# Optimization experiments

Hardware: AMD Instinct MI355X
Metric: run time of the kernel (lower is better)

The kernel has to match this reference:

```python
import jax, jax.numpy as jnp
import numpy as np

B, T, E, H = 2, 2048, 1024, 16
D = E // H          # head_size = 64
DF = 4 * E          # FFN inner dim


def setup_inputs() -> dict:
    key = jax.random.key(0)
    ks = jax.random.split(key, 10)
    s = E ** -0.5
    return {
        "x":  jax.random.normal(ks[0], (B, T, E), jnp.float32),
        "Wq": jax.random.normal(ks[1], (H, E, D), jnp.float32) * s,
        "Wk": jax.random.normal(ks[2], (H, E, D), jnp.float32) * s,
        "Wv": jax.random.normal(ks[3], (H, E, D), jnp.float32) * s,
        "Wo": jax.random.normal(ks[4], (E, E), jnp.float32) * s,
        "bo": jnp.zeros((E,), jnp.float32),
        "W1": jax.random.normal(ks[5], (E, DF), jnp.float32) * s,
        "b1": jnp.zeros((DF,), jnp.float32),
        "W2": jax.random.normal(ks[6], (DF, E), jnp.float32) * (DF ** -0.5),
        "b2": jnp.zeros((E,), jnp.float32),
    }


def reference(x, Wq, Wk, Wv, Wo, bo, W1, b1, W2, b2):
    Bx, Tx, C = x.shape
    # NOTE: source scales by C**-0.5 where C = n_embed (not head_size) -- faithful.
    scale = C ** -0.5
    q = jnp.einsum('btc,hcd->bhtd', x, Wq)
    k = jnp.einsum('btc,hcd->bhtd', x, Wk)
    v = jnp.einsum('btc,hcd->bhtd', x, Wv)
    scores = jnp.einsum('bhtd,bhsd->bhts', q, k) * scale   # [B,H,T,T]
    causal = jnp.tril(jnp.ones((Tx, Tx), bool))
    scores = jnp.where(causal, scores, -jnp.inf)
    attn = jax.nn.softmax(scores, axis=-1)
    out = jnp.einsum('bhts,bhsd->bhtd', attn, v)
    out = out.transpose(0, 2, 1, 3).reshape(Bx, Tx, C)     # concat heads
    x = x + (out @ Wo + bo)                                # residual + projection
    h = jax.nn.relu(x @ W1 + b1)
    x = x + (h @ W2 + b2)                                  # residual + FFN
    return x
```

## Files before the change

### kernel.cpp

```cpp
#include <hip/hip_runtime.h>

#define B_ 2
#define T_ 2048
#define E_ 1024
#define H_ 16
#define D_ 64
#define DF_ 4096
#define M_ (B_*T_)
#define NQKV_ 3072

typedef unsigned short u16;
typedef __attribute__((ext_vector_type(8))) short short8;
typedef __attribute__((ext_vector_type(4))) float f32x4;
typedef __attribute__((ext_vector_type(16))) float f32x16;

__device__ __forceinline__ u16 f2bf(float f) {
  unsigned u = __builtin_bit_cast(unsigned, f);
  u += 0x7FFFu + ((u >> 16) & 1u);
  return (u16)(u >> 16);
}
__device__ __forceinline__ unsigned cvtpk(float a, float b) {
  unsigned r;
  asm("v_cvt_pk_bf16_f32 %0, %1, %2" : "=v"(r) : "v"(a), "v"(b));
  return r;
}
__device__ __forceinline__ float exp2a(float x) {
  float r;
  asm("v_exp_f32 %0, %1" : "=v"(r) : "v"(x));
  return r;
}
__device__ __forceinline__ float bf2f(u16 u) {
  return __builtin_bit_cast(float, (unsigned)u << 16);
}
__device__ __forceinline__ float vmax16(const f32x16& v) {
  float a0 = fmaxf(v[0], v[1]),   a1 = fmaxf(v[2], v[3]);
  float a2 = fmaxf(v[4], v[5]),   a3 = fmaxf(v[6], v[7]);
  float a4 = fmaxf(v[8], v[9]),   a5 = fmaxf(v[10], v[11]);
  float a6 = fmaxf(v[12], v[13]), a7 = fmaxf(v[14], v[15]);
  float b0 = fmaxf(a0, a1), b1 = fmaxf(a2, a3), b2 = fmaxf(a4, a5), b3 = fmaxf(a6, a7);
  return fmaxf(fmaxf(b0, b1), fmaxf(b2, b3));
}
__device__ __forceinline__ float vsum16(const f32x16& v) {
  float a0 = v[0] + v[1],   a1 = v[2] + v[3];
  float a2 = v[4] + v[5],   a3 = v[6] + v[7];
  float a4 = v[8] + v[9],   a5 = v[10] + v[11];
  float a6 = v[12] + v[13], a7 = v[14] + v[15];
  float b0 = a0 + a1, b1 = a2 + a3, b2 = a4 + a5, b3 = a6 + a7;
  return (b0 + b1) + (b2 + b3);
}

__device__ __forceinline__ void gload_lds16(const u16* g, u16* l) {
  __builtin_amdgcn_global_load_lds((const __attribute__((address_space(1))) void*)g,
                                   (__attribute__((address_space(3))) void*)l, 16, 0, 0);
}

__global__ __launch_bounds__(256) void cast_bf16_kernel(const float* __restrict__ in,
                                                        u16* __restrict__ out, int n4) {
  int i = blockIdx.x * 256 + threadIdx.x;
  if (i >= n4) return;
  float4 v = ((const float4*)in)[i];
  uint2 r;
  r.x = cvtpk(v.x, v.y);
  r.y = cvtpk(v.z, v.w);
  ((uint2*)out)[i] = r;
}

__global__ __launch_bounds__(256) void transpose_cast_kernel(const float* __restrict__ in,
                                                             u16* __restrict__ out,
                                                             int R, int C, int outld) {
  __shared__ float tile[32][33];
  int z = blockIdx.z;
  int c0 = blockIdx.x * 32, r0 = blockIdx.y * 32;
  int tx = threadIdx.x & 31, ty = threadIdx.x >> 5;
  const float* ip = in + (size_t)z * R * C;
#pragma unroll
  for (int i = 0; i < 32; i += 8)
    tile[ty + i][tx] = ip[(size_t)(r0 + ty + i) * C + (c0 + tx)];
  __syncthreads();
#pragma unroll
  for (int i = 0; i < 32; i += 8)
    out[(size_t)(z * C + c0 + ty + i) * outld + (r0 + tx)] = f2bf(tile[tx][ty + i]);
}

template<int TM, int TN, bool BIAS, bool RELU, bool RES, bool OF32, bool OBF, bool VSPLIT>
__global__ __launch_bounds__(256, 2)
void gemm_bt(const u16* __restrict__ A,
             const u16* __restrict__ Bt,
             int M, int N, int K, int lda, int ldb,
             const float* __restrict__ bias,
             const float* __restrict__ res,
             float* __restrict__ outf,
             u16* __restrict__ outb,
             u16* __restrict__ vtb) {
  constexpr int MF = TM / 32;
  constexpr int NF = TN / 32;
  constexpr int ACH = TM / 32;
  constexpr int BCH = TN / 32;
  __shared__ __attribute__((aligned(16))) u16 As[2][TM][64];
  __shared__ __attribute__((aligned(16))) u16 Bs[2][TN][64];
  int m0 = blockIdx.y * TM, n0 = blockIdx.x * TN;
  int z = blockIdx.z;
  A  += (size_t)z * K;
  Bt += (size_t)z * K;
  if (OF32 && outf) outf += (size_t)z * M * N;
  if (OBF && outb)  outb += (size_t)z * M * N;
  int tid = threadIdx.x;
  int lane = tid & 63, w = tid >> 6;
  int wr = w >> 1, wc = w & 1;
  int lg = lane >> 4, lq = lane & 15;
  int srow8 = lane >> 3;
  int scolsw = ((lane & 7) ^ srow8) * 8;

  const u16* aSrcP[ACH];
  const u16* bSrcP[BCH];
#pragma unroll
  for (int j = 0; j < ACH; j++)
    aSrcP[j] = &A[(size_t)(m0 + w * (ACH * 8) + j * 8 + srow8) * lda + scolsw];
#pragma unroll
  for (int j = 0; j < BCH; j++)
    bSrcP[j] = &Bt[(size_t)(n0 + w * (BCH * 8) + j * 8 + srow8) * ldb + scolsw];

  auto stage = [&](int buf, int k0) {
#pragma unroll
    for (int j = 0; j < ACH; j++)
      gload_lds16(aSrcP[j] + k0, &As[buf][w * (ACH * 8) + j * 8][0]);
#pragma unroll
    for (int j = 0; j < BCH; j++)
      gload_lds16(bSrcP[j] + k0, &Bs[buf][w * (BCH * 8) + j * 8][0]);
  };

  f32x4 acc[MF][NF] = {};
  int lqx = lq & 7;

  stage(0, 0);
  __syncthreads();
  int cur = 0;
  for (int k0 = 0; k0 < K; k0 += 64) {
    if (k0 + 64 < K) stage(cur ^ 1, k0 + 64);
#pragma unroll
    for (int kk = 0; kk < 2; kk++) {
      short8 af[MF], bf[NF];
      int csw = ((lg + kk * 4) ^ lqx) * 8;
#pragma unroll
      for (int m = 0; m < MF; m++) af[m] = *(const short8*)&As[cur][wr * (TM / 2) + m * 16 + lq][csw];
#pragma unroll
      for (int n = 0; n < NF; n++) bf[n] = *(const short8*)&Bs[cur][wc * (TN / 2) + n * 16 + lq][csw];
#pragma unroll
      for (int m = 0; m < MF; m++)
#pragma unroll
        for (int n = 0; n < NF; n++)
          acc[m][n] = __builtin_amdgcn_mfma_f32_16x16x32_bf16(af[m], bf[n], acc[m][n], 0, 0, 0);
    }
    __syncthreads();
    cur ^= 1;
  }

#pragma unroll
  for (int m = 0; m < MF; m++)
#pragma unroll
    for (int n = 0; n < NF; n++) {
      int row = m0 + wr * (TM / 2) + m * 16 + lg * 4;
      int col = n0 + wc * (TN / 2) + n * 16 + lq;
      float bv = BIAS ? bias[col] : 0.f;
      float vv[4];
#pragma unroll
      for (int r = 0; r < 4; r++) {
        float v = acc[m][n][r];
        if (BIAS) v += bv;
        if (RES)  v += res[(size_t)(row + r) * N + col];
        if (RELU) v = fmaxf(v, 0.f);
        if (OF32) outf[(size_t)(row + r) * N + col] = v;
        vv[r] = v;
      }
      if (OBF) {
        unsigned p01 = cvtpk(vv[0], vv[1]);
        unsigned p23 = cvtpk(vv[2], vv[3]);
        if (VSPLIT && n0 >= 2048) {
          uint2 rr; rr.x = p01; rr.y = p23;
          *(uint2*)&vtb[(size_t)(col - 2048) * M + row] = rr;
        } else {
          outb[(size_t)(row + 0) * N + col] = (u16)p01;
          outb[(size_t)(row + 1) * N + col] = (u16)(p01 >> 16);
          outb[(size_t)(row + 2) * N + col] = (u16)p23;
          outb[(size_t)(row + 3) * N + col] = (u16)(p23 >> 16);
        }
      }
    }
}

__global__ __launch_bounds__(256) void reduce2_kernel(const float* __restrict__ x1,
                                                      const u16* __restrict__ p0,
                                                      const u16* __restrict__ p1,
                                                      const float* __restrict__ b2,
                                                      float* __restrict__ out) {
  int i = blockIdx.x * 256 + threadIdx.x;
  float4 xv = ((const float4*)x1)[i];
  ushort4 a = ((const ushort4*)p0)[i];
  ushort4 b = ((const ushort4*)p1)[i];
  const float4 bb = *(const float4*)&b2[(i * 4) & (E_ - 1)];
  float4 r;
  r.x = xv.x + bf2f(a.x) + bf2f(b.x) + bb.x;
  r.y = xv.y + bf2f(a.y) + bf2f(b.y) + bb.y;
  r.z = xv.z + bf2f(a.z) + bf2f(b.z) + bb.z;
  r.w = xv.w + bf2f(a.w) + bf2f(b.w) + bb.w;
  ((float4*)out)[i] = r;
}

__global__ __launch_bounds__(512, 4) void attn_kernel(const u16* __restrict__ qkv,
                                                      const u16* __restrict__ Vt,
                                                      u16* __restrict__ attn) {
  __shared__ __attribute__((aligned(16))) u16 Ks[2][64 * 64];
  __shared__ __attribute__((aligned(16))) u16 Vs[2][64 * 64];
  __shared__ float ml[4][2][32];
  int bid = blockIdx.x;
  int pp = bid >> 8, rrb = bid & 255;
  int h  = rrb >> 4;
  int jj = rrb & 15;
  int b  = pp;
  int qt = pp ? (15 - jj) : jj;
  int tid = threadIdx.x;
  int lane = tid & 63, w = tid >> 6;
  int qg = w & 3;
  int par = w >> 2;
  int l31 = lane & 31, hh = lane >> 5;
  int q0w = qt * 128 + qg * 32;
  int q_abs = q0w + l31;

  short8 qf[4];
  const u16* Qrow = qkv + (size_t)(b * T_ + q_abs) * NQKV_ + h * 64;
#pragma unroll
  for (int ks = 0; ks < 4; ks++) qf[ks] = *(const short8*)&Qrow[ks * 16 + hh * 8];

  const u16* Kbase  = qkv + (size_t)(b * T_) * NQKV_ + 1024 + h * 64;
  const u16* Vtbase = Vt + (size_t)(h * 64) * M_ + b * T_;

  int r0s = tid >> 3, c0s = tid & 7;
  unsigned kd0 = (unsigned)((r0s * 128 + c0s * 16) ^ ((r0s & 7) << 4));
  const u16* Kg0 = &Kbase[(size_t)r0s * NQKV_ + c0s * 8];
  const u16* Vg0 = &Vtbase[(size_t)r0s * M_ + c0s * 8];

  f32x16 o[2] = {};
  float m_run = -__builtin_inff(), l_run = 0.f;
  const float SCL2 = 0.045084223f;
  const int s_stop = qt * 128 + 128;

  uint4 kr0 = *(const uint4*)Kg0;
  uint4 vr0 = *(const uint4*)Vg0;
  *(uint4*)((char*)&Ks[0][0] + kd0) = kr0;
  *(uint4*)((char*)&Vs[0][0] + kd0) = vr0;
  kr0 = *(const uint4*)&Kg0[(size_t)64 * NQKV_];
  vr0 = *(const uint4*)&Vg0[64];
  __syncthreads();
  int cur = 0;

  for (int s0 = 0; s0 < s_stop; s0 += 64) {
    if (s0 + 64 < s_stop) {
      *(uint4*)((char*)&Ks[cur ^ 1][0] + kd0) = kr0;
      *(uint4*)((char*)&Vs[cur ^ 1][0] + kd0) = vr0;
      if (s0 + 128 < s_stop) {
        kr0 = *(const uint4*)&Kg0[(size_t)(s0 + 128) * NQKV_];
        vr0 = *(const uint4*)&Vg0[s0 + 128];
      }
    }

    if (((s0 >> 6) & 1) == par && s0 <= q0w + 31) {
      const char* KsC = (const char*)&Ks[cur][0];
      const char* VsC = (const char*)&Vs[cur][0];

      f32x16 st[2];
      __builtin_amdgcn_s_setprio(1);
#pragma unroll
      for (int c = 0; c < 2; c++) {
        f32x16 acc = {};
        int key = c * 32 + l31;
#pragma unroll
        for (int ks = 0; ks < 4; ks++) {
          unsigned off = (unsigned)((key * 128 + ks * 32 + hh * 16) ^ ((key & 7) << 4));
          short8 kf = *(const short8*)(KsC + off);
          acc = __builtin_amdgcn_mfma_f32_32x32x16_bf16(kf, qf[ks], acc, 0, 0, 0);
        }
        st[c] = acc;
      }
      __builtin_amdgcn_s_setprio(0);

      if (s0 + 63 > q0w) {
#pragma unroll
        for (int c = 0; c < 2; c++)
#pragma unroll
          for (int r = 0; r < 16; r++) {
            int key = s0 + c * 32 + (r & 3) + 8 * (r >> 2) + 4 * hh;
            st[c][r] = (key > q_abs) ? -__builtin_inff() : st[c][r];
          }
      }
      float tmax = fmaxf(vmax16(st[0]), vmax16(st[1]));
      tmax = fmaxf(tmax, __shfl_xor(tmax, 32));

      if (!__all(tmax - m_run <= 256.0f)) {
        float newm = fmaxf(m_run, tmax);
        float fac = exp2a((m_run - newm) * SCL2);
        l_run *= fac;
        o[0] *= fac;
        o[1] *= fac;
        m_run = newm;
      }
      float nm2 = -m_run * SCL2;
#pragma unroll
      for (int c = 0; c < 2; c++)
#pragma unroll
        for (int r = 0; r < 16; r++)
          st[c][r] = exp2a(fmaf(st[c][r], SCL2, nm2));
      float psum = vsum16(st[0]) + vsum16(st[1]);
      psum += __shfl_xor(psum, 32);
      l_run += psum;

      unsigned wds[2][8];
#pragma unroll
      for (int c = 0; c < 2; c++)
#pragma unroll
        for (int i = 0; i < 8; i++)
          wds[c][i] = cvtpk(st[c][2 * i], st[c][2 * i + 1]);

      __builtin_amdgcn_s_setprio(1);
#pragma unroll
      for (int ks16 = 0; ks16 < 4; ks16++) {
        int c = ks16 >> 1, e = ks16 & 1;
        unsigned send0 = hh ? wds[c][4 * e]     : wds[c][4 * e + 2];
        unsigned send1 = hh ? wds[c][4 * e + 1] : wds[c][4 * e + 3];
        unsigned recv0 = (unsigned)__shfl_xor((int)send0, 32);
        unsigned recv1 = (unsigned)__shfl_xor((int)send1, 32);
        uint4 fw;
        fw.x = hh ? recv0 : wds[c][4 * e];
        fw.y = hh ? recv1 : wds[c][4 * e + 1];
        fw.z = hh ? wds[c][4 * e + 2] : recv0;
        fw.w = hh ? wds[c][4 * e + 3] : recv1;
        short8 pf = __builtin_bit_cast(short8, fw);
#pragma unroll
        for (int dc = 0; dc < 2; dc++) {
          int d = dc * 32 + l31;
          unsigned off = (unsigned)((d * 128 + ks16 * 32 + hh * 16) ^ ((d & 7) << 4));
          short8 vf = *(const short8*)(VsC + off);
          o[dc] = __builtin_amdgcn_mfma_f32_32x32x16_bf16(vf, pf, o[dc], 0, 0, 0);
        }
      }
      __builtin_amdgcn_s_setprio(0);
    }

    __syncthreads();
    cur ^= 1;
  }

  if (w >= 4) {
    char* mb = (w < 6) ? ((char*)&Ks[0][0] + (w - 4) * 8192)
                       : ((char*)&Vs[0][0] + (w - 6) * 8192);
#pragma unroll
    for (int g = 0; g < 8; g++) {
      float4 v4;
      v4.x = o[g >> 2][(g & 3) * 4];
      v4.y = o[g >> 2][(g & 3) * 4 + 1];
      v4.z = o[g >> 2][(g & 3) * 4 + 2];
      v4.w = o[g >> 2][(g & 3) * 4 + 3];
      *(float4*)(mb + g * 1024 + lane * 16) = v4;
    }
    if (hh == 0) {
      ml[qg][0][l31] = m_run;
      ml[qg][1][l31] = l_run;
    }
  }
  __syncthreads();
  if (w < 4) {
    const char* mb = (qg < 2) ? ((const char*)&Ks[0][0] + qg * 8192)
                              : ((const char*)&Vs[0][0] + (qg - 2) * 8192);
    float m1 = ml[qg][0][l31];
    float l1 = ml[qg][1][l31];
    float mn = fmaxf(m_run, m1);
    float f0 = exp2a((m_run - mn) * SCL2);
    float f1 = exp2a((m1 - mn) * SCL2);
    float ln = l_run * f0 + l1 * f1;
    float inv = 1.f / ln;
    float g0 = f0 * inv, g1 = f1 * inv;
    const size_t orow = (size_t)(b * T_ + q_abs) * E_ + h * 64;
#pragma unroll
    for (int g = 0; g < 8; g++) {
      float4 o1 = *(const float4*)(mb + g * 1024 + lane * 16);
      int dc = g >> 2, a = g & 3;
      float e0 = o[dc][4 * a]     * g0 + o1.x * g1;
      float e1 = o[dc][4 * a + 1] * g0 + o1.y * g1;
      float e2 = o[dc][4 * a + 2] * g0 + o1.z * g1;
      float e3 = o[dc][4 * a + 3] * g0 + o1.w * g1;
      uint2 r;
      r.x = cvtpk(e0, e1);
      r.y = cvtpk(e2, e3);
      *(uint2*)&attn[orow + dc * 32 + 8 * a + 4 * hh] = r;
    }
  }
}

extern "C" void kernel_launch(void* const* d_in, const int* in_sizes, int n_in,
                              void* d_out, int out_size, void* d_ws, size_t ws_size,
                              hipStream_t stream) {
  const float* x  = (const float*)d_in[0];
  const float* Wq = (const float*)d_in[1];
  const float* Wk = (const float*)d_in[2];
  const float* Wv = (const float*)d_in[3];
  const float* Wo = (const float*)d_in[4];
  const float* bo = (const float*)d_in[5];
  const float* W1 = (const float*)d_in[6];
  const float* b1 = (const float*)d_in[7];
  const float* W2 = (const float*)d_in[8];
  const float* b2 = (const float*)d_in[9];
  float* out = (float*)d_out;

  const size_t MB = 1048576;
  char* ws = (char*)d_ws;
  u16* xb    = (u16*)(ws + 0);
  u16* WqkvT = (u16*)(ws + 8 * MB);
  u16* WoT   = (u16*)(ws + 14 * MB);
  u16* W1T   = (u16*)(ws + 16 * MB);
  u16* W2T   = (u16*)(ws + 24 * MB);
  u16* qkv   = (u16*)(ws + 32 * MB);
  u16* attn  = (u16*)(ws + 56 * MB);
  float* x1  = (float*)(ws + 64 * MB);
  u16* Vtb   = (u16*)(ws + 64 * MB);
  u16* x1b   = (u16*)(ws + 0);
  u16* hbuf  = (u16*)(ws + 32 * MB);
  u16* pbuf  = (u16*)(ws + 0);

  cast_bf16_kernel<<<(M_ * E_ / 4 + 255) / 256, 256, 0, stream>>>(x, xb, M_ * E_ / 4);
  transpose_cast_kernel<<<dim3(2, 32, 16),  256, 0, stream>>>(Wq, WqkvT,                E_, D_, E_);
  transpose_cast_kernel<<<dim3(2, 32, 16),  256, 0, stream>>>(Wk, WqkvT + 1024 * 1024,  E_, D_, E_);
  transpose_cast_kernel<<<dim3(2, 32, 16),  256, 0, stream>>>(Wv, WqkvT + 2048 * 1024,  E_, D_, E_);
  transpose_cast_kernel<<<dim3(32, 32, 1),  256, 0, stream>>>(Wo, WoT, E_, E_, E_);
  transpose_cast_kernel<<<dim3(128, 32, 1), 256, 0, stream>>>(W1, W1T, E_, DF_, E_);
  transpose_cast_kernel<<<dim3(32, 128, 1), 256, 0, stream>>>(W2, W2T, DF_, E_, DF_);

  gemm_bt<128,128,false,false,false,false,true,true><<<dim3(NQKV_ / 128, M_ / 128), 256, 0, stream>>>(
      xb, WqkvT, M_, NQKV_, E_, E_, E_, nullptr, nullptr, nullptr, qkv, Vtb);

  attn_kernel<<<B_ * H_ * (T_ / 128), 512, 0, stream>>>(qkv, Vtb, attn);

  gemm_bt<64,128,true,false,true,true,true,false><<<dim3(E_ / 128, M_ / 64), 256, 0, stream>>>(
      attn, WoT, M_, E_, E_, E_, E_, bo, x, x1, x1b, nullptr);
  gemm_bt<128,128,true,true,false,false,true,false><<<dim3(DF_ / 128, M_ / 128), 256, 0, stream>>>(
      x1b, W1T, M_, DF_, E_, E_, E_, b1, nullptr, nullptr, hbuf, nullptr);
  gemm_bt<128,128,false,false,false,false,true,false><<<dim3(E_ / 128, M_ / 128, 2), 256, 0, stream>>>(
      hbuf, W2T, M_, E_, DF_ / 2, DF_, DF_, nullptr, nullptr, nullptr, pbuf, nullptr);
  reduce2_kernel<<<M_ * E_ / 4 / 256, 256, 0, stream>>>(x1, pbuf, pbuf + (size_t)M_ * E_, b2, out);
}
```

Measured before the change: 226.3 us.

## Split attention KV range four ways per 64-query tile with tree merge

```diff
diff --git a/kernel.cpp b/kernel.cpp
--- a/kernel.cpp
+++ b/kernel.cpp
@@ -211,19 +211,19 @@
                                                       u16* __restrict__ attn) {
   __shared__ __attribute__((aligned(16))) u16 Ks[2][64 * 64];
   __shared__ __attribute__((aligned(16))) u16 Vs[2][64 * 64];
-  __shared__ float ml[4][2][32];
+  __shared__ float ml[8][2][32];
   int bid = blockIdx.x;
-  int pp = bid >> 8, rrb = bid & 255;
-  int h  = rrb >> 4;
-  int jj = rrb & 15;
+  int pp = bid >> 9, rrb = bid & 511;
+  int h  = rrb >> 5;
+  int jj = rrb & 31;
   int b  = pp;
-  int qt = pp ? (15 - jj) : jj;
+  int qt = pp ? (31 - jj) : jj;
   int tid = threadIdx.x;
   int lane = tid & 63, w = tid >> 6;
-  int qg = w & 3;
-  int par = w >> 2;
+  int qg = w & 1;
+  int par = w >> 1;
   int l31 = lane & 31, hh = lane >> 5;
-  int q0w = qt * 128 + qg * 32;
+  int q0w = qt * 64 + qg * 32;
   int q_abs = q0w + l31;
 
   short8 qf[4];
@@ -242,7 +242,7 @@
   f32x16 o[2] = {};
   float m_run = -__builtin_inff(), l_run = 0.f;
   const float SCL2 = 0.045084223f;
-  const int s_stop = qt * 128 + 128;
+  const int s_stop = qt * 64 + 64;
 
   uint4 kr0 = *(const uint4*)Kg0;
   uint4 vr0 = *(const uint4*)Vg0;
@@ -263,7 +263,7 @@
       }
     }
 
-    if (((s0 >> 6) & 1) == par && s0 <= q0w + 31) {
+    if (((s0 >> 6) & 3) == par && s0 <= q0w + 31) {
       const char* KsC = (const char*)&Ks[cur][0];
       const char* VsC = (const char*)&Vs[cur][0];
 
@@ -349,9 +349,7 @@
     cur ^= 1;
   }
 
-  if (w >= 4) {
-    char* mb = (w < 6) ? ((char*)&Ks[0][0] + (w - 4) * 8192)
-                       : ((char*)&Vs[0][0] + (w - 6) * 8192);
+  auto spill = [&](char* mb) {
 #pragma unroll
     for (int g = 0; g < 8; g++) {
       float4 v4;
@@ -361,37 +359,59 @@
       v4.w = o[g >> 2][(g & 3) * 4 + 3];
       *(float4*)(mb + g * 1024 + lane * 16) = v4;
     }
-    if (hh == 0) {
-      ml[qg][0][l31] = m_run;
-      ml[qg][1][l31] = l_run;
-    }
-  }
-  __syncthreads();
-  if (w < 4) {
-    const char* mb = (qg < 2) ? ((const char*)&Ks[0][0] + qg * 8192)
-                              : ((const char*)&Vs[0][0] + (qg - 2) * 8192);
-    float m1 = ml[qg][0][l31];
-    float l1 = ml[qg][1][l31];
+    if (hh == 0) { ml[w][0][l31] = m_run; ml[w][1][l31] = l_run; }
+  };
+  auto merge = [&](const char* mb, int pw) {
+    float m1 = ml[pw][0][l31], l1 = ml[pw][1][l31];
     float mn = fmaxf(m_run, m1);
-    float f0 = exp2a((m_run - mn) * SCL2);
-    float f1 = exp2a((m1 - mn) * SCL2);
-    float ln = l_run * f0 + l1 * f1;
-    float inv = 1.f / ln;
-    float g0 = f0 * inv, g1 = f1 * inv;
-    const size_t orow = (size_t)(b * T_ + q_abs) * E_ + h * 64;
+    float f0, f1;
+    if (mn == -__builtin_inff()) { f0 = 1.f; f1 = 0.f; }
+    else {
+      f0 = exp2a((m_run - mn) * SCL2);
+      f1 = exp2a((m1 - mn) * SCL2);
+    }
 #pragma unroll
     for (int g = 0; g < 8; g++) {
       float4 o1 = *(const float4*)(mb + g * 1024 + lane * 16);
       int dc = g >> 2, a = g & 3;
-      float e0 = o[dc][4 * a]     * g0 + o1.x * g1;
-      float e1 = o[dc][4 * a + 1] * g0 + o1.y * g1;
-      float e2 = o[dc][4 * a + 2] * g0 + o1.z * g1;
-      float e3 = o[dc][4 * a + 3] * g0 + o1.w * g1;
-      uint2 r;
-      r.x = cvtpk(e0, e1);
-      r.y = cvtpk(e2, e3);
-      *(uint2*)&attn[orow + dc * 32 + 8 * a + 4 * hh] = r;
-    }
+      o[dc][4 * a]     = o[dc][4 * a]     * f0 + o1.x * f1;
+      o[dc][4 * a + 1] = o[dc][4 * a + 1] * f0 + o1.y * f1;
+      o[dc][4 * a + 2] = o[dc][4 * a + 2] * f0 + o1.z * f1;
+      o[dc][4 * a + 3] = o[dc][4 * a + 3] * f0 + o1.w * f1;
+    }
+    l_run = l_run * f0 + l1 * f1;
+    m_run = mn;
+  };
+
+  if (w >= 4) {
+    char* mb = (w < 6) ? ((char*)&Ks[0][0] + (w - 4) * 8192)
+                       : ((char*)&Vs[0][0] + (w - 6) * 8192);
+    spill(mb);
+  }
+  __syncthreads();
+  if (w < 4) {
+    const char* mb = (w < 2) ? ((const char*)&Ks[0][0] + w * 8192)
+                             : ((const char*)&Vs[0][0] + (w - 2) * 8192);
+    merge(mb, w + 4);
+  }
+  __syncthreads();
+  if (w == 2 || w == 3) spill((char*)&Ks[0][0] + (w - 2) * 8192);
+  __syncthreads();
+  if (w < 2) {
+    merge((const char*)&Ks[0][0] + w * 8192, w + 2);
+    float inv = 1.f / l_run;
+    const size_t orow = (size_t)(b * T_ + q_abs) * E_ + h * 64;
+#pragma unroll
+    for (int dc = 0; dc < 2; dc++)
+#pragma unroll
+      for (int a = 0; a < 4; a++) {
+        float e0 = o[dc][4 * a] * inv,     e1 = o[dc][4 * a + 1] * inv;
+        float e2 = o[dc][4 * a + 2] * inv, e3 = o[dc][4 * a + 3] * inv;
+        uint2 r;
+        r.x = cvtpk(e0, e1);
+        r.y = cvtpk(e2, e3);
+        *(uint2*)&attn[orow + dc * 32 + 8 * a + 4 * hh] = r;
+      }
   }
 }
 
@@ -436,7 +456,7 @@
   gemm_bt<128,128,false,false,false,false,true,true><<<dim3(NQKV_ / 128, M_ / 128), 256, 0, stream>>>(
       xb, WqkvT, M_, NQKV_, E_, E_, E_, nullptr, nullptr, nullptr, qkv, Vtb);
 
-  attn_kernel<<<B_ * H_ * (T_ / 128), 512, 0, stream>>>(qkv, Vtb, attn);
+  attn_kernel<<<B_ * H_ * (T_ / 64), 512, 0, stream>>>(qkv, Vtb, attn);
 
   gemm_bt<64,128,true,false,true,true,true,false><<<dim3(E_ / 128, M_ / 64), 256, 0, stream>>>(
       attn, WoT, M_, E_, E_, E_, E_, bo, x, x1, x1b, nullptr);
```

New measurement: 263.2 us. 1.16x slower.
